# Optimization experiments

Hardware: AMD Instinct MI355X
Metric: run time of the kernel (lower is better)

The kernel has to match this reference:

```python
import jax, jax.numpy as jnp
import numpy as np

HIDDEN = 2048
NUM_HEADS = 16
HEAD_DIM = HIDDEN // NUM_HEADS
ROPE_THETA = 10000.0


def _rope_cos_sin(n, dtype):
    # Llama-style: inv_freq over even indices, emb = concat([freqs, freqs])
    inv_freq = 1.0 / (ROPE_THETA ** (jnp.arange(0, HEAD_DIM, 2, dtype=jnp.float32) / HEAD_DIM))
    pos = jnp.arange(n, dtype=jnp.float32)
    freqs = pos[:, None] * inv_freq[None, :]          # [N, HEAD_DIM/2]
    emb = jnp.concatenate([freqs, freqs], axis=-1)    # [N, HEAD_DIM]
    return jnp.cos(emb).astype(dtype), jnp.sin(emb).astype(dtype)


def _rotate_half(x):
    x1, x2 = jnp.split(x, 2, axis=-1)
    return jnp.concatenate([-x2, x1], axis=-1)


def setup_inputs() -> dict:
    key = jax.random.key(0)
    ks = jax.random.split(key, 5)
    B, N, D = 2, 2048, HIDDEN
    s = 1.0 / np.sqrt(D)
    return {
        "x": jax.random.normal(ks[0], (B, N, D), jnp.float32),
        "Wq": jax.random.normal(ks[1], (D, D), jnp.float32) * s,
        "Wk": jax.random.normal(ks[2], (D, D), jnp.float32) * s,
        "Wv": jax.random.normal(ks[3], (D, D), jnp.float32) * s,
        "Wo": jax.random.normal(ks[4], (D, D), jnp.float32) * s,
    }


def reference(x, Wq, Wk, Wv, Wo):
    B, N, D = x.shape
    scale = HEAD_DIM ** -0.5

    def proj(W):  # nn.Linear(bias=False): x @ W.T, then split heads -> [B,H,N,hd]
        return (x @ W.T).reshape(B, N, NUM_HEADS, HEAD_DIM).transpose(0, 2, 1, 3)

    q, k, v = proj(Wq), proj(Wk), proj(Wv)

    cos, sin = _rope_cos_sin(N, x.dtype)  # [N, HEAD_DIM]
    cos = cos[None, None]                 # broadcast over B, H
    sin = sin[None, None]
    q = q * cos + _rotate_half(q) * sin
    k = k * cos + _rotate_half(k) * sin

    attn = jnp.einsum("bhqd,bhkd->bhqk", q, k) * scale  # full N x N scores
    attn = jax.nn.softmax(attn, axis=-1)                 # dropout p=0 -> identity
    out = jnp.einsum("bhqk,bhkd->bhqd", attn, v)
    out = out.transpose(0, 2, 1, 3).reshape(B, N, D)
    return out @ Wo.T
```

## Files before the change

kernel.cpp:

```cpp
#include <hip/hip_runtime.h>
#include <hip/hip_bf16.h>
#include <math.h>

typedef short bf16x8 __attribute__((ext_vector_type(8)));
typedef short bf16x4 __attribute__((ext_vector_type(4)));
typedef float f32x4 __attribute__((ext_vector_type(4)));

#define NSEQ 2048
#define DMODEL 2048
#define NH 16
#define HD 128
#define BATCH 2
#define MROWS 4096

__device__ __forceinline__ unsigned short f2b(float f) {
    __hip_bfloat16 h = __float2bfloat16(f);
    return *reinterpret_cast<unsigned short*>(&h);
}
__device__ __forceinline__ float b2f(unsigned short u) {
    __hip_bfloat16 h;
    *reinterpret_cast<unsigned short*>(&h) = u;
    return __bfloat162float(h);
}

__device__ __forceinline__ void gld_lds16(const unsigned short* g, unsigned short* l) {
    __builtin_amdgcn_global_load_lds(
        (const __attribute__((address_space(1))) unsigned int*)(const void*)g,
        (__attribute__((address_space(3))) unsigned int*)(void*)l,
        16, 0, 0);
}

__global__ __launch_bounds__(256) void cast_all_kernel(const float* __restrict__ x,
                                                       const float* __restrict__ wq,
                                                       const float* __restrict__ wk,
                                                       const float* __restrict__ wv,
                                                       const float* __restrict__ wo,
                                                       unsigned short* __restrict__ xb,
                                                       unsigned short* __restrict__ wqb) {
    int bid = blockIdx.x;
    const float* src;
    unsigned short* dst;
    int off;
    if (bid < 4096) {
        src = x; dst = xb; off = bid;
    } else {
        int w = (bid - 4096) >> 11;
        src = (w == 0) ? wq : (w == 1) ? wk : (w == 2) ? wv : wo;
        dst = wqb + (size_t)w * 4194304;
        off = (bid - 4096) & 2047;
    }
    int i = (off * 256 + threadIdx.x) * 8;
    float4 a = *(const float4*)(src + i);
    float4 b = *(const float4*)(src + i + 4);
    union { unsigned short u[8]; uint4 v; } tmp;
    tmp.u[0] = f2b(a.x); tmp.u[1] = f2b(a.y); tmp.u[2] = f2b(a.z); tmp.u[3] = f2b(a.w);
    tmp.u[4] = f2b(b.x); tmp.u[5] = f2b(b.y); tmp.u[6] = f2b(b.z); tmp.u[7] = f2b(b.w);
    *(uint4*)(dst + i) = tmp.v;
}

__global__ __launch_bounds__(256) void gemm_qkv(const unsigned short* __restrict__ A,
                                                const unsigned short* __restrict__ Bw,
                                                unsigned short* __restrict__ qk,
                                                unsigned short* __restrict__ vt) {
    __shared__ unsigned short sA[128 * 32];
    __shared__ unsigned short sB[128 * 32];
    const int K = DMODEL;
    const int tid = threadIdx.x;
    const int wave = tid >> 6, lane = tid & 63;
    const int m0 = blockIdx.y * 128, n0 = blockIdx.x * 128;
    const int wm = wave * 32;

    f32x4 acc[2][8] = {};

    const int srow = wave * 32 + (lane >> 2);
    const int scol = (lane & 3) * 8;
    const unsigned short* Ag = A + (size_t)(m0 + srow) * K + scol;
    const unsigned short* Bg = Bw + (size_t)(n0 + srow) * K + scol;
    unsigned short* sA0 = &sA[(wave * 32) * 32];
    unsigned short* sA1 = &sA[(wave * 32 + 16) * 32];
    unsigned short* sB0 = &sB[(wave * 32) * 32];
    unsigned short* sB1 = &sB[(wave * 32 + 16) * 32];
    const int fr = lane & 15, fo = (lane >> 4) * 8;

    for (int kb = 0; kb < K; kb += 32) {
        gld_lds16(Ag + kb, sA0);
        gld_lds16(Ag + (size_t)16 * K + kb, sA1);
        gld_lds16(Bg + kb, sB0);
        gld_lds16(Bg + (size_t)16 * K + kb, sB1);
        __syncthreads();
        bf16x8 af[2], bfr[8];
        #pragma unroll
        for (int mt = 0; mt < 2; mt++)
            af[mt] = *(const bf16x8*)&sA[(wm + mt * 16 + fr) * 32 + fo];
        #pragma unroll
        for (int nt = 0; nt < 8; nt++)
            bfr[nt] = *(const bf16x8*)&sB[(nt * 16 + fr) * 32 + fo];
        #pragma unroll
        for (int mt = 0; mt < 2; mt++)
            #pragma unroll
            for (int nt = 0; nt < 8; nt++)
                acc[mt][nt] = __builtin_amdgcn_mfma_f32_16x16x32_bf16(af[mt], bfr[nt], acc[mt][nt], 0, 0, 0);
        __syncthreads();
    }

    const int g4 = (lane >> 4) * 4, c0 = lane & 15;
    if (n0 < 4096) {
        const float scale = (n0 < 2048) ? 0.08838834764831845f : 1.0f;
        unsigned short* dst = qk + (size_t)(n0 >> 11) * 8388608;
        const int colbase = n0 & 2047;
        float invf[4];
        #pragma unroll
        for (int nt = 0; nt < 4; nt++)
            invf[nt] = exp2f((float)(nt * 16 + c0) * -0.2076205059304545f);
        #pragma unroll
        for (int mt = 0; mt < 2; mt++) {
            #pragma unroll
            for (int r = 0; r < 4; r++) {
                int row = m0 + wm + mt * 16 + g4 + r;
                float nf = (float)(row & (NSEQ - 1));
                size_t rbase = (size_t)row * 2048 + colbase + c0;
                #pragma unroll
                for (int nt = 0; nt < 4; nt++) {
                    float sv, cv;
                    __sincosf(nf * invf[nt], &sv, &cv);
                    float lo = acc[mt][nt][r], hi = acc[mt][nt + 4][r];
                    dst[rbase + nt * 16]      = f2b((lo * cv - hi * sv) * scale);
                    dst[rbase + nt * 16 + 64] = f2b((hi * cv + lo * sv) * scale);
                }
            }
        }
    } else {
        #pragma unroll
        for (int mt = 0; mt < 2; mt++) {
            int mbase = m0 + wm + mt * 16 + g4;
            int bb = mbase >> 11;
            int nn = mbase & 2047;
            #pragma unroll
            for (int nt = 0; nt < 8; nt++) {
                int d = n0 - 4096 + nt * 16 + c0;
                union { unsigned short u[4]; uint2 v; } o;
                #pragma unroll
                for (int r = 0; r < 4; r++) o.u[r] = f2b(acc[mt][nt][r]);
                *(uint2*)(vt + ((size_t)(bb * 2048 + d)) * 2048 + nn) = o.v;
            }
        }
    }
}

__global__ __launch_bounds__(256) void gemm_out(const unsigned short* __restrict__ A,
                                                const unsigned short* __restrict__ Bw,
                                                float* __restrict__ Cf) {
    __shared__ unsigned short sA[128 * 64];
    __shared__ unsigned short sB[128 * 64];
    const int K = DMODEL, Nn = DMODEL;
    const int tid = threadIdx.x;
    const int wave = tid >> 6, lane = tid & 63;
    const int m0 = blockIdx.y * 128, n0 = blockIdx.x * 128;
    const int wm = (wave >> 1) * 64, wn = (wave & 1) * 64;

    f32x4 acc[4][4] = {};

    const int srowoff = wave * 8 + (lane >> 3);
    const int gchunk = ((lane & 7) ^ ((lane >> 3) & 7)) * 8;
    const unsigned short* Ag = A + (size_t)(m0 + srowoff) * K + gchunk;
    const unsigned short* Bg = Bw + (size_t)(n0 + srowoff) * K + gchunk;
    unsigned short* sAw = &sA[(wave * 8) * 64];
    unsigned short* sBw = &sB[(wave * 8) * 64];

    const int fr = lane & 15, grp = lane >> 4;
    const int swz = fr & 7;

    for (int kb = 0; kb < K; kb += 64) {
        #pragma unroll
        for (int i = 0; i < 4; i++)
            gld_lds16(Ag + (size_t)(i * 32) * K + kb, sAw + i * 32 * 64);
        #pragma unroll
        for (int i = 0; i < 4; i++)
            gld_lds16(Bg + (size_t)(i * 32) * K + kb, sBw + i * 32 * 64);
        __syncthreads();
        #pragma unroll
        for (int ks = 0; ks < 2; ks++) {
            bf16x8 af[4], bfr[4];
            #pragma unroll
            for (int mt = 0; mt < 4; mt++)
                af[mt] = *(const bf16x8*)&sA[(wm + mt * 16 + fr) * 64 + (((ks * 4 + grp) ^ swz) << 3)];
            #pragma unroll
            for (int nt = 0; nt < 4; nt++)
                bfr[nt] = *(const bf16x8*)&sB[(wn + nt * 16 + fr) * 64 + (((ks * 4 + grp) ^ swz) << 3)];
            #pragma unroll
            for (int mt = 0; mt < 4; mt++)
                #pragma unroll
                for (int nt = 0; nt < 4; nt++)
                    acc[mt][nt] = __builtin_amdgcn_mfma_f32_16x16x32_bf16(af[mt], bfr[nt], acc[mt][nt], 0, 0, 0);
        }
        __syncthreads();
    }

    const int g4 = (lane >> 4) * 4, c0 = lane & 15;
    #pragma unroll
    for (int mt = 0; mt < 4; mt++)
        #pragma unroll
        for (int nt = 0; nt < 4; nt++) {
            int col = n0 + wn + nt * 16 + c0;
            #pragma unroll
            for (int r = 0; r < 4; r++) {
                int row = m0 + wm + mt * 16 + g4 + r;
                Cf[(size_t)row * Nn + col] = acc[mt][nt][r];
            }
        }
}

__global__ __launch_bounds__(256) void attn_kernel(const unsigned short* __restrict__ Q,
                                                   const unsigned short* __restrict__ Kg,
                                                   const unsigned short* __restrict__ Vt,
                                                   unsigned short* __restrict__ O) {
    __shared__ unsigned short sK[64 * 136];
    __shared__ unsigned short sV[128 * 88];

    const int bh = blockIdx.x;
    const int b = bh >> 4, h = bh & 15;
    const int qt = blockIdx.y;
    const int tid = threadIdx.x, wave = tid >> 6, lane = tid & 63;
    const int c0 = lane & 15, grp = lane >> 4;

    bf16x8 qf[2][4];
    {
        const unsigned short* Qbase = Q + (size_t)(b * NSEQ + qt * 128 + wave * 32 + c0) * DMODEL + h * HD + grp * 8;
        #pragma unroll
        for (int nt = 0; nt < 2; nt++)
            #pragma unroll
            for (int ks = 0; ks < 4; ks++)
                qf[nt][ks] = *(const bf16x8*)(Qbase + (size_t)nt * 16 * DMODEL + ks * 32);
    }

    f32x4 oacc[8][2] = {};
    float lsum[2] = {0.f, 0.f};

    const unsigned short* Kbase = Kg + (size_t)(b * NSEQ) * DMODEL + h * HD;
    const unsigned short* Vbase = Vt + (size_t)(bh * HD) * NSEQ;

    for (int kv0 = 0; kv0 < NSEQ; kv0 += 64) {
        __syncthreads();
        #pragma unroll
        for (int i = 0; i < 4; i++) {
            int fl = i * 256 + tid;
            int rr = fl >> 4, cc = fl & 15;
            *(uint4*)&sK[rr * 136 + cc * 8] = *(const uint4*)(Kbase + (size_t)(kv0 + rr) * DMODEL + cc * 8);
        }
        #pragma unroll
        for (int i = 0; i < 4; i++) {
            int fl = i * 256 + tid;
            int rr = fl >> 3, cc = fl & 7;
            *(uint4*)&sV[rr * 88 + cc * 8] = *(const uint4*)(Vbase + (size_t)rr * NSEQ + kv0 + cc * 8);
        }
        __syncthreads();

        f32x4 s[4][2] = {};
        #pragma unroll
        for (int ks = 0; ks < 4; ks++) {
            bf16x8 kf[4];
            #pragma unroll
            for (int mt = 0; mt < 4; mt++)
                kf[mt] = *(const bf16x8*)&sK[(mt * 16 + c0) * 136 + ks * 32 + grp * 8];
            #pragma unroll
            for (int mt = 0; mt < 4; mt++)
                #pragma unroll
                for (int nt = 0; nt < 2; nt++)
                    s[mt][nt] = __builtin_amdgcn_mfma_f32_16x16x32_bf16(kf[mt], qf[nt][ks], s[mt][nt], 0, 0, 0);
        }

        bf16x4 pk[4][2];
        #pragma unroll
        for (int mt = 0; mt < 4; mt++)
            #pragma unroll
            for (int nt = 0; nt < 2; nt++) {
                float p0 = __expf(s[mt][nt][0]);
                float p1 = __expf(s[mt][nt][1]);
                float p2 = __expf(s[mt][nt][2]);
                float p3 = __expf(s[mt][nt][3]);
                lsum[nt] += (p0 + p1) + (p2 + p3);
                bf16x4 t;
                t[0] = (short)f2b(p0); t[1] = (short)f2b(p1);
                t[2] = (short)f2b(p2); t[3] = (short)f2b(p3);
                pk[mt][nt] = t;
            }

        #pragma unroll
        for (int mtK = 0; mtK < 4; mtK++) {
            bf16x4 va[8];
            #pragma unroll
            for (int mo = 0; mo < 8; mo++)
                va[mo] = *(const bf16x4*)&sV[(mo * 16 + c0) * 88 + mtK * 16 + grp * 4];
            #pragma unroll
            for (int mo = 0; mo < 8; mo++)
                #pragma unroll
                for (int nt = 0; nt < 2; nt++)
                    oacc[mo][nt] = __builtin_amdgcn_mfma_f32_16x16x16bf16_1k(va[mo], pk[mtK][nt], oacc[mo][nt], 0, 0, 0);
        }
    }

    float invl[2];
    #pragma unroll
    for (int nt = 0; nt < 2; nt++) {
        float li = lsum[nt];
        li += __shfl_xor(li, 16);
        li += __shfl_xor(li, 32);
        invl[nt] = 1.0f / li;
    }
    #pragma unroll
    for (int mo = 0; mo < 8; mo++)
        #pragma unroll
        for (int nt = 0; nt < 2; nt++) {
            union { unsigned short u[4]; uint2 v; } o;
            #pragma unroll
            for (int r = 0; r < 4; r++)
                o.u[r] = f2b(oacc[mo][nt][r] * invl[nt]);
            int row = b * NSEQ + qt * 128 + wave * 32 + nt * 16 + c0;
            int col = h * HD + mo * 16 + grp * 4;
            *(uint2*)(O + (size_t)row * DMODEL + col) = o.v;
        }
}

extern "C" void kernel_launch(void* const* d_in, const int* in_sizes, int n_in,
                              void* d_out, int out_size, void* d_ws, size_t ws_size,
                              hipStream_t stream) {
    const float* x  = (const float*)d_in[0];
    const float* Wq = (const float*)d_in[1];
    const float* Wk = (const float*)d_in[2];
    const float* Wv = (const float*)d_in[3];
    const float* Wo = (const float*)d_in[4];

    char* ws = (char*)d_ws;
    unsigned short* xb  = (unsigned short*)(ws);
    unsigned short* wqb = (unsigned short*)(ws + 16777216);
    unsigned short* wob = (unsigned short*)(ws + 16777216 + 3 * 8388608);
    unsigned short* qb  = (unsigned short*)(ws + 50331648);
    unsigned short* kb  = (unsigned short*)(ws + 67108864);
    unsigned short* vt  = (unsigned short*)(ws + 83886080);

    cast_all_kernel<<<12288, 256, 0, stream>>>(x, Wq, Wk, Wv, Wo, xb, wqb);

    gemm_qkv<<<dim3(48, 32), 256, 0, stream>>>(xb, wqb, qb, vt);

    attn_kernel<<<dim3(32, 16), 256, 0, stream>>>(qb, kb, vt, xb);

    gemm_out<<<dim3(16, 32), 256, 0, stream>>>(xb, wob, (float*)d_out);
}
```

Baseline: 384.8 us.

## Rewrite QKV GEMM with 256x256 tiles, 4-stage LDS pipeline and swizzle

Rewrites the QKV projection GEMM to use 512-thread blocks computing 256x256 output tiles, with a 4-slot LDS ring buffer prefetching three k-steps ahead via async global-to-LDS loads. It uses explicit waitcnt and barriers, XOR-swizzled LDS addressing to avoid bank conflicts, a grouped block-index swizzle for L2 reuse, and raised wave priority around the MFMA bursts. The RoPE and V-transpose epilogue is remapped to the new per-wave fragment layout. This aims to hide global load latency and raise MFMA utilization, in exchange for much more LDS per block (64 KB), more accumulator registers and fragile hand-written sync.

Result: slower. 401.9 us (+4.4%).

```diff
diff --git a/kernel.cpp b/kernel.cpp
--- a/kernel.cpp
+++ b/kernel.cpp
@@ -58,86 +58,138 @@
     *(uint4*)(dst + i) = tmp.v;
 }
 
-__global__ __launch_bounds__(256) void gemm_qkv(const unsigned short* __restrict__ A,
-                                                const unsigned short* __restrict__ Bw,
-                                                unsigned short* __restrict__ qk,
-                                                unsigned short* __restrict__ vt) {
-    __shared__ unsigned short sA[128 * 32];
-    __shared__ unsigned short sB[128 * 32];
+__global__ __launch_bounds__(512, 2) void gemm_qkv(const unsigned short* __restrict__ A,
+                                                   const unsigned short* __restrict__ Bw,
+                                                   unsigned short* __restrict__ qk,
+                                                   unsigned short* __restrict__ vt) {
+    __shared__ unsigned short sA[4][8192];
+    __shared__ unsigned short sB[4][8192];
     const int K = DMODEL;
     const int tid = threadIdx.x;
     const int wave = tid >> 6, lane = tid & 63;
-    const int m0 = blockIdx.y * 128, n0 = blockIdx.x * 128;
-    const int wm = wave * 32;
-
-    f32x4 acc[2][8] = {};
-
-    const int srow = wave * 32 + (lane >> 2);
-    const int scol = (lane & 3) * 8;
-    const unsigned short* Ag = A + (size_t)(m0 + srow) * K + scol;
-    const unsigned short* Bg = Bw + (size_t)(n0 + srow) * K + scol;
-    unsigned short* sA0 = &sA[(wave * 32) * 32];
-    unsigned short* sA1 = &sA[(wave * 32 + 16) * 32];
-    unsigned short* sB0 = &sB[(wave * 32) * 32];
-    unsigned short* sB1 = &sB[(wave * 32 + 16) * 32];
-    const int fr = lane & 15, fo = (lane >> 4) * 8;
-
-    for (int kb = 0; kb < K; kb += 32) {
-        gld_lds16(Ag + kb, sA0);
-        gld_lds16(Ag + (size_t)16 * K + kb, sA1);
-        gld_lds16(Bg + kb, sB0);
-        gld_lds16(Bg + (size_t)16 * K + kb, sB1);
-        __syncthreads();
-        bf16x8 af[2], bfr[8];
-        #pragma unroll
-        for (int mt = 0; mt < 2; mt++)
-            af[mt] = *(const bf16x8*)&sA[(wm + mt * 16 + fr) * 32 + fo];
-        #pragma unroll
-        for (int nt = 0; nt < 8; nt++)
-            bfr[nt] = *(const bf16x8*)&sB[(nt * 16 + fr) * 32 + fo];
-        #pragma unroll
-        for (int mt = 0; mt < 2; mt++)
-            #pragma unroll
-            for (int nt = 0; nt < 8; nt++)
-                acc[mt][nt] = __builtin_amdgcn_mfma_f32_16x16x32_bf16(af[mt], bfr[nt], acc[mt][nt], 0, 0, 0);
-        __syncthreads();
-    }
-
-    const int g4 = (lane >> 4) * 4, c0 = lane & 15;
+
+    const int bid = blockIdx.x;
+    const int swz = (bid & 7) * 48 + (bid >> 3);
+    const int m0 = (swz & 15) * 256;
+    const int n0 = (swz >> 4) * 256;
+
+    const int wr = wave >> 2, wc = wave & 3;
+    const int fr = lane & 15, grp = lane >> 4;
+    const int rsw = (grp ^ ((fr >> 1) & 3)) << 3;
+
+    const int sr = wave * 16 + (lane >> 2);
+    const int sc = (((lane & 3) ^ ((lane >> 3) & 3)) << 3);
+    const unsigned short* Ag = A + (size_t)(m0 + sr) * K + sc;
+    const unsigned short* Bg = Bw + (size_t)(n0 + sr) * K + sc;
+
+    f32x4 acc[8][4] = {};
+
+    #pragma unroll
+    for (int t = 0; t < 3; t++) {
+        #pragma unroll
+        for (int i = 0; i < 2; i++) {
+            gld_lds16(Ag + (size_t)(i * 128) * K + t * 32, &sA[t][(i * 128 + wave * 16) * 32]);
+            gld_lds16(Bg + (size_t)(i * 128) * K + t * 32, &sB[t][(i * 128 + wave * 16) * 32]);
+        }
+    }
+    __builtin_amdgcn_sched_barrier(0);
+    asm volatile("s_waitcnt vmcnt(8)" ::: "memory");
+    asm volatile("s_barrier" ::: "memory");
+
+    const int arow = (wr * 128 + fr) * 32 + rsw;
+    const int brow = (wc * 16 + fr) * 32 + rsw;
+
+    for (int s = 0; s < 64; s++) {
+        const int slot = s & 3;
+        const unsigned short* aS = sA[slot];
+        const unsigned short* bS = sB[slot];
+
+        bf16x8 afA[4], bfr[4];
+        #pragma unroll
+        for (int mt = 0; mt < 4; mt++)
+            afA[mt] = *(const bf16x8*)&aS[arow + mt * 512];
+        #pragma unroll
+        for (int nt = 0; nt < 4; nt++)
+            bfr[nt] = *(const bf16x8*)&bS[brow + ((nt & 1) * 64 + (nt >> 1) * 128) * 32];
+        if (s < 61) {
+            const int t = s + 3, slw = t & 3;
+            #pragma unroll
+            for (int i = 0; i < 2; i++)
+                gld_lds16(Ag + (size_t)(i * 128) * K + t * 32, &sA[slw][(i * 128 + wave * 16) * 32]);
+        }
+        __builtin_amdgcn_sched_barrier(0);
+        asm volatile("s_barrier" ::: "memory");
+        asm volatile("s_waitcnt lgkmcnt(0)" ::: "memory");
+        __builtin_amdgcn_sched_barrier(0);
+        __builtin_amdgcn_s_setprio(1);
+        #pragma unroll
+        for (int mt = 0; mt < 4; mt++)
+            #pragma unroll
+            for (int nt = 0; nt < 4; nt++)
+                acc[mt][nt] = __builtin_amdgcn_mfma_f32_16x16x32_bf16(afA[mt], bfr[nt], acc[mt][nt], 0, 0, 0);
+        __builtin_amdgcn_s_setprio(0);
+        __builtin_amdgcn_sched_barrier(0);
+        asm volatile("s_barrier" ::: "memory");
+
+        bf16x8 afB[4];
+        #pragma unroll
+        for (int mt = 0; mt < 4; mt++)
+            afB[mt] = *(const bf16x8*)&aS[arow + (mt + 4) * 512];
+        if (s < 61) {
+            const int t = s + 3, slw = t & 3;
+            #pragma unroll
+            for (int i = 0; i < 2; i++)
+                gld_lds16(Bg + (size_t)(i * 128) * K + t * 32, &sB[slw][(i * 128 + wave * 16) * 32]);
+        }
+        __builtin_amdgcn_sched_barrier(0);
+        asm volatile("s_barrier" ::: "memory");
+        asm volatile("s_waitcnt lgkmcnt(0)" ::: "memory");
+        __builtin_amdgcn_sched_barrier(0);
+        __builtin_amdgcn_s_setprio(1);
+        #pragma unroll
+        for (int mt = 0; mt < 4; mt++)
+            #pragma unroll
+            for (int nt = 0; nt < 4; nt++)
+                acc[mt + 4][nt] = __builtin_amdgcn_mfma_f32_16x16x32_bf16(afB[mt], bfr[nt], acc[mt + 4][nt], 0, 0, 0);
+        __builtin_amdgcn_s_setprio(0);
+        __builtin_amdgcn_sched_barrier(0);
+        if (s < 61)       asm volatile("s_waitcnt vmcnt(8)" ::: "memory");
+        else if (s == 61) asm volatile("s_waitcnt vmcnt(4)" ::: "memory");
+        else if (s == 62) asm volatile("s_waitcnt vmcnt(0)" ::: "memory");
+        asm volatile("s_barrier" ::: "memory");
+    }
+
+    const int g4 = grp * 4, c0 = fr;
     if (n0 < 4096) {
         const float scale = (n0 < 2048) ? 0.08838834764831845f : 1.0f;
         unsigned short* dst = qk + (size_t)(n0 >> 11) * 8388608;
-        const int colbase = n0 & 2047;
-        float invf[4];
-        #pragma unroll
-        for (int nt = 0; nt < 4; nt++)
-            invf[nt] = exp2f((float)(nt * 16 + c0) * -0.2076205059304545f);
-        #pragma unroll
-        for (int mt = 0; mt < 2; mt++) {
+        const int colbase = (n0 & 2047) + wc * 16 + c0;
+        const float inv = exp2f((float)(wc * 16 + c0) * -0.2076205059304545f);
+        #pragma unroll
+        for (int mt = 0; mt < 8; mt++) {
             #pragma unroll
             for (int r = 0; r < 4; r++) {
-                int row = m0 + wm + mt * 16 + g4 + r;
+                int row = m0 + wr * 128 + mt * 16 + g4 + r;
                 float nf = (float)(row & (NSEQ - 1));
-                size_t rbase = (size_t)row * 2048 + colbase + c0;
-                #pragma unroll
-                for (int nt = 0; nt < 4; nt++) {
-                    float sv, cv;
-                    __sincosf(nf * invf[nt], &sv, &cv);
-                    float lo = acc[mt][nt][r], hi = acc[mt][nt + 4][r];
-                    dst[rbase + nt * 16]      = f2b((lo * cv - hi * sv) * scale);
-                    dst[rbase + nt * 16 + 64] = f2b((hi * cv + lo * sv) * scale);
-                }
+                float sv, cv;
+                __sincosf(nf * inv, &sv, &cv);
+                size_t rbase = (size_t)row * 2048 + colbase;
+                float lo0 = acc[mt][0][r], hi0 = acc[mt][1][r];
+                dst[rbase]       = f2b((lo0 * cv - hi0 * sv) * scale);
+                dst[rbase + 64]  = f2b((hi0 * cv + lo0 * sv) * scale);
+                float lo1 = acc[mt][2][r], hi1 = acc[mt][3][r];
+                dst[rbase + 128] = f2b((lo1 * cv - hi1 * sv) * scale);
+                dst[rbase + 192] = f2b((hi1 * cv + lo1 * sv) * scale);
             }
         }
     } else {
         #pragma unroll
-        for (int mt = 0; mt < 2; mt++) {
-            int mbase = m0 + wm + mt * 16 + g4;
-            int bb = mbase >> 11;
-            int nn = mbase & 2047;
-            #pragma unroll
-            for (int nt = 0; nt < 8; nt++) {
-                int d = n0 - 4096 + nt * 16 + c0;
+        for (int mt = 0; mt < 8; mt++) {
+            int row0 = m0 + wr * 128 + mt * 16 + g4;
+            int bb = row0 >> 11, nn = row0 & 2047;
+            #pragma unroll
+            for (int nt = 0; nt < 4; nt++) {
+                int d = (n0 - 4096) + (nt & 1) * 64 + (nt >> 1) * 128 + wc * 16 + c0;
                 union { unsigned short u[4]; uint2 v; } o;
                 #pragma unroll
                 for (int r = 0; r < 4; r++) o.u[r] = f2b(acc[mt][nt][r]);
@@ -340,9 +392,9 @@
 
     cast_all_kernel<<<12288, 256, 0, stream>>>(x, Wq, Wk, Wv, Wo, xb, wqb);
 
-    gemm_qkv<<<dim3(48, 32), 256, 0, stream>>>(xb, wqb, qb, vt);
+    gemm_qkv<<<384, 512, 0, stream>>>(xb, wqb, qb, vt);
 
     attn_kernel<<<dim3(32, 16), 256, 0, stream>>>(qb, kb, vt, xb);
 
-    gemm_out<<<dim3(16, 32), 256, 0, stream>>>(xb, wob, (float*)d_out);
-}
+    gemm_out<<<16 * 32 > 512 ? dim3(16, 32) : dim3(16, 32), 256, 0, stream>>>(xb, wob, (float*)d_out);
+}
```

## Double-buffer attention K/V tiles with direct global-to-LDS loads and XOR swizzle

Applied to the files above, without the earlier changes.

The attention kernel now double-buffers its K and V tiles in shared memory. It prefetches the next 64-key tile with direct global-to-LDS loads while the current tile is computed, which replaces the two-barrier load-then-compute loop. Padding is replaced by an XOR swizzle to avoid bank conflicts, and block indices are remapped so that blocks sharing a head are spread across the grid. LDS use roughly doubles, which may reduce occupancy, and correctness depends on gld_lds16 semantics and on the swizzle matching between writes and reads.

Measured after the change: 380.8 us. No clear change (-1.0%).

```diff
diff --git a/kernel.cpp b/kernel.cpp
--- a/kernel.cpp
+++ b/kernel.cpp
@@ -214,12 +214,14 @@
                                                    const unsigned short* __restrict__ Kg,
                                                    const unsigned short* __restrict__ Vt,
                                                    unsigned short* __restrict__ O) {
-    __shared__ unsigned short sK[64 * 136];
-    __shared__ unsigned short sV[128 * 88];
-
-    const int bh = blockIdx.x;
+    __shared__ unsigned short sK[2][64 * 128];
+    __shared__ unsigned short sV[2][128 * 64];
+
+    const int lin = blockIdx.x;
+    const int swz = (lin & 7) * 64 + (lin >> 3);
+    const int qt = swz & 15;
+    const int bh = swz >> 4;
     const int b = bh >> 4, h = bh & 15;
-    const int qt = blockIdx.y;
     const int tid = threadIdx.x, wave = tid >> 6, lane = tid & 63;
     const int c0 = lane & 15, grp = lane >> 4;
 
@@ -239,21 +241,35 @@
     const unsigned short* Kbase = Kg + (size_t)(b * NSEQ) * DMODEL + h * HD;
     const unsigned short* Vbase = Vt + (size_t)(bh * HD) * NSEQ;
 
-    for (int kv0 = 0; kv0 < NSEQ; kv0 += 64) {
-        __syncthreads();
-        #pragma unroll
-        for (int i = 0; i < 4; i++) {
-            int fl = i * 256 + tid;
-            int rr = fl >> 4, cc = fl & 15;
-            *(uint4*)&sK[rr * 136 + cc * 8] = *(const uint4*)(Kbase + (size_t)(kv0 + rr) * DMODEL + cc * 8);
-        }
-        #pragma unroll
-        for (int i = 0; i < 4; i++) {
-            int fl = i * 256 + tid;
-            int rr = fl >> 3, cc = fl & 7;
-            *(uint4*)&sV[rr * 88 + cc * 8] = *(const uint4*)(Vbase + (size_t)rr * NSEQ + kv0 + cc * 8);
-        }
-        __syncthreads();
+    #define ATTN_STAGE(bi, kv0)                                                        \
+        {                                                                              \
+            _Pragma("unroll")                                                          \
+            for (int i = 0; i < 4; i++) {                                              \
+                int rr = wave * 16 + i * 4 + (lane >> 4);                              \
+                int gc = ((lane & 15) ^ (rr & 15)) * 8;                                \
+                gld_lds16(Kbase + (size_t)((kv0) + rr) * DMODEL + gc,                  \
+                          &sK[bi][(wave * 16 + i * 4) * 128]);                         \
+            }                                                                          \
+            _Pragma("unroll")                                                          \
+            for (int i = 0; i < 4; i++) {                                              \
+                int rr = wave * 32 + i * 8 + (lane >> 3);                              \
+                int gc = ((lane & 7) ^ (lane >> 3)) * 8;                               \
+                gld_lds16(Vbase + (size_t)rr * NSEQ + (kv0) + gc,                      \
+                          &sV[bi][(wave * 32 + i * 8) * 64]);                          \
+            }                                                                          \
+        }
+
+    ATTN_STAGE(0, 0);
+    __syncthreads();
+
+    for (int it = 0; it < 32; it++) {
+        const unsigned short* sKb = sK[it & 1];
+        const unsigned short* sVb = sV[it & 1];
+
+        if (it < 31) {
+            ATTN_STAGE((it + 1) & 1, (it + 1) * 64);
+        }
+        __builtin_amdgcn_sched_barrier(0);
 
         f32x4 s[4][2] = {};
         #pragma unroll
@@ -261,7 +277,7 @@
             bf16x8 kf[4];
             #pragma unroll
             for (int mt = 0; mt < 4; mt++)
-                kf[mt] = *(const bf16x8*)&sK[(mt * 16 + c0) * 136 + ks * 32 + grp * 8];
+                kf[mt] = *(const bf16x8*)&sKb[(mt * 16 + c0) * 128 + (((ks * 4 + grp) ^ c0) << 3)];
             #pragma unroll
             for (int mt = 0; mt < 4; mt++)
                 #pragma unroll
@@ -290,13 +306,17 @@
             bf16x4 va[8];
             #pragma unroll
             for (int mo = 0; mo < 8; mo++)
-                va[mo] = *(const bf16x4*)&sV[(mo * 16 + c0) * 88 + mtK * 16 + grp * 4];
+                va[mo] = *(const bf16x4*)&sVb[(mo * 16 + c0) * 64
+                                              + (((mtK * 2 + (grp >> 1)) ^ (c0 & 7)) << 3)
+                                              + (grp & 1) * 4];
             #pragma unroll
             for (int mo = 0; mo < 8; mo++)
                 #pragma unroll
                 for (int nt = 0; nt < 2; nt++)
                     oacc[mo][nt] = __builtin_amdgcn_mfma_f32_16x16x16bf16_1k(va[mo], pk[mtK][nt], oacc[mo][nt], 0, 0, 0);
         }
+
+        __syncthreads();
     }
 
     float invl[2];
@@ -342,7 +362,7 @@
 
     gemm_qkv<<<dim3(48, 32), 256, 0, stream>>>(xb, wqb, qb, vt);
 
-    attn_kernel<<<dim3(32, 16), 256, 0, stream>>>(qb, kb, vt, xb);
+    attn_kernel<<<512, 256, 0, stream>>>(qb, kb, vt, xb);
 
     gemm_out<<<dim3(16, 32), 256, 0, stream>>>(xb, wob, (float*)d_out);
 }
```
